# Kernel tuning notes

Measured on AMD Instinct MI355X. Metric: run time of the kernel, lower is better.

Reference implementation:

```python
import jax, jax.numpy as jnp
import numpy as np

N, E, D, H = 50000, 800000, 128, 4
DH = D // H
BN_EPS = 1e-5


def setup_inputs() -> dict:
    key = jax.random.key(0)
    ks = jax.random.split(key, 16)
    s = 0.02
    inp = {
        "x": jax.random.normal(ks[0], (N, D), dtype=jnp.float32),
        "edge_index": jax.random.randint(ks[1], (2, E), 0, N, dtype=jnp.int64),
        "Wk": jax.random.normal(ks[2], (D, D), dtype=jnp.float32) * s,
        "bk": jnp.zeros((D,), jnp.float32),
        "Wm": jax.random.normal(ks[3], (D, D), dtype=jnp.float32) * s,
        "bm": jnp.zeros((D,), jnp.float32),
        "Wq": jax.random.normal(ks[4], (D, D), dtype=jnp.float32) * s,
        "bq": jnp.zeros((D,), jnp.float32),
        "W1": jax.random.normal(ks[5], (D, D), dtype=jnp.float32) * s,
        "b1": jnp.zeros((D,), jnp.float32),
        "gamma": jnp.ones((D,), jnp.float32),
        "beta": jnp.zeros((D,), jnp.float32),
        "W2": jax.random.normal(ks[6], (D, D), dtype=jnp.float32) * s,
        "b2": jnp.zeros((D,), jnp.float32),
    }
    return inp


def reference(x, edge_index, Wk, bk, Wm, bm, Wq, bq, W1, b1, gamma, beta, W2, b2):
    src = edge_index[0]  # [E] softmax segment key
    dst = edge_index[1]  # [E] aggregation target
    x_i = x[dst]         # [E, D] (torch code: X[1])
    x_j = x[src]         # [E, D] (torch code: X[0])

    key = (x_i @ Wk + bk).reshape(-1, H, DH)
    msg = (x_j @ Wm + bm).reshape(-1, H, DH)
    query = (x_j @ Wq + bq).reshape(-1, H, DH) / jnp.sqrt(jnp.float32(DH))

    scores = jnp.sum(query * key, axis=2)  # [E, H]

    # segment softmax over src node index (numerically stable)
    smax = jax.ops.segment_max(scores, src, num_segments=N)
    e = jnp.exp(scores - smax[src])
    ssum = jax.ops.segment_sum(e, src, num_segments=N)
    alpha = e / ssum[src]  # [E, H]

    # rescale by per-src-node edge count
    cnt = jax.ops.segment_sum(jnp.ones((scores.shape[0],), jnp.float32), src, num_segments=N)
    alpha = alpha * cnt[src][:, None]

    out_e = (msg * alpha[:, :, None]).reshape(-1, D)  # [E, D]
    out = jax.ops.segment_sum(out_e, dst, num_segments=N)  # [N, D]

    # MLP: Linear -> BatchNorm1d (training-mode batch stats) -> ReLU -> Linear
    h = out @ W1 + b1
    mean = jnp.mean(h, axis=0)
    var = jnp.var(h, axis=0)  # biased variance, as torch BN uses for normalization
    h = (h - mean) * jax.lax.rsqrt(var + BN_EPS) * gamma + beta
    h = jax.nn.relu(h)
    return h @ W2 + b2
```

## Files before the change

kernel.cpp:

```cpp
#include <hip/hip_runtime.h>
#include <hip/hip_bf16.h>

#define N_NODES 50000
#define N_EDGES 800000
#define DIM 128
#define NHEAD 4
#define GEMM_BLOCKS 782
#define RANK_ILP 8
#define RANK_BLOCKS 391

typedef __bf16 bf16x8 __attribute__((ext_vector_type(8)));
typedef __bf16 bf16x2 __attribute__((ext_vector_type(2)));
typedef float f32x4 __attribute__((ext_vector_type(4)));

struct WPtrs { const float* w[5]; };

__global__ __launch_bounds__(256) void prep_weights(WPtrs P, __bf16* __restrict__ Wt)
{
  __shared__ __bf16 tileT[16][136];
  const int mat = blockIdx.x >> 3, sl = blockIdx.x & 7;
  const float* W = P.w[mat];
  const int col0 = sl * 16;
  const int t = threadIdx.x;
  #pragma unroll
  for (int i = 0; i < 8; ++i) {
    int id = t + i * 256;
    int k = id >> 4, c = id & 15;
    tileT[c][k] = (__bf16)W[k * 128 + col0 + c];
  }
  __syncthreads();
  int c = t >> 4, kb = t & 15;
  bf16x8 v = *(const bf16x8*)&tileT[c][kb * 8];
  *(bf16x8*)&Wt[(size_t)mat * 16384 + (size_t)(col0 + c) * 128 + kb * 8] = v;
}


__device__ __forceinline__ void stage_Wt_half(const __bf16* __restrict__ Wt,
    int half, __bf16 (*wLDS)[136])
{
  const int t = threadIdx.x;
  const __bf16* base = Wt + (size_t)half * 64 * 128;
  #pragma unroll
  for (int i = 0; i < 4; ++i) {
    int id = t + i * 256;
    int col = id >> 4, kb = id & 15;
    bf16x8 v = ((const bf16x8*)(base + (size_t)col * 128))[kb];
    *(bf16x8*)&wLDS[col][kb * 8] = v;
  }
}

__device__ __forceinline__ void stage_A_f32(const float* __restrict__ A, int row0,
    int nrows, __bf16 (*aLDS)[136])
{
  const int t = threadIdx.x;
  #pragma unroll
  for (int i = 0; i < 4; ++i) {
    int id = t + i * 256;
    int r = id >> 4, cb = id & 15;
    int gr = row0 + r;
    float4 v0 = make_float4(0.f, 0.f, 0.f, 0.f), v1 = v0;
    if (gr < nrows) {
      const float4* row = (const float4*)(A + (size_t)gr * DIM);
      v0 = row[cb * 2];
      v1 = row[cb * 2 + 1];
    }
    bf16x8 o;
    o[0] = (__bf16)v0.x; o[1] = (__bf16)v0.y; o[2] = (__bf16)v0.z; o[3] = (__bf16)v0.w;
    o[4] = (__bf16)v1.x; o[5] = (__bf16)v1.y; o[6] = (__bf16)v1.z; o[7] = (__bf16)v1.w;
    *(bf16x8*)&aLDS[r][cb * 8] = o;
  }
}

__device__ __forceinline__ void stage_A_bf16(const __bf16* __restrict__ A, int row0,
    int nrows, __bf16 (*aLDS)[136])
{
  const int t = threadIdx.x;
  #pragma unroll
  for (int i = 0; i < 4; ++i) {
    int id = t + i * 256;
    int r = id >> 4, cb = id & 15;
    int gr = row0 + r;
    bf16x8 v = {};
    if (gr < nrows) v = ((const bf16x8*)(A + (size_t)gr * DIM))[cb];
    *(bf16x8*)&aLDS[r][cb * 8] = v;
  }
}

__device__ __forceinline__ void mfma_half(const __bf16 (*aLDS)[136],
    const __bf16 (*wLDS)[136], int half, f32x4 acc[8])
{
  const int lane = threadIdx.x & 63, wave = threadIdx.x >> 6;
  const int m = lane & 15, q = lane >> 4;
  #pragma unroll
  for (int kt = 0; kt < 4; ++kt) {
    bf16x8 a = *(const bf16x8*)&aLDS[wave * 16 + m][kt * 32 + q * 8];
    #pragma unroll
    for (int ct = 0; ct < 4; ++ct) {
      bf16x8 b = *(const bf16x8*)&wLDS[ct * 16 + m][kt * 32 + q * 8];
      acc[half * 4 + ct] =
          __builtin_amdgcn_mfma_f32_16x16x32_bf16(a, b, acc[half * 4 + ct], 0, 0, 0);
    }
  }
}

template <typename OutT>
__device__ __forceinline__ void store_tile(f32x4 acc[8],
    const float* __restrict__ bias, float scale, OutT* __restrict__ C,
    int row0, int nrows)
{
  const int lane = threadIdx.x & 63, wave = threadIdx.x >> 6;
  const int m = lane & 15, q = lane >> 4;
  #pragma unroll
  for (int j = 0; j < 8; ++j) {
    int col = (j >> 2) * 64 + (j & 3) * 16 + m;
    float bv = bias[col];
    #pragma unroll
    for (int r = 0; r < 4; ++r) {
      int row = row0 + wave * 16 + q * 4 + r;
      if (row < nrows) C[(size_t)row * DIM + col] = (OutT)((acc[j][r] + bv) * scale);
    }
  }
}

__device__ __forceinline__ void gemm_pass(const __bf16 (*aLDS)[136],
    __bf16 (*wLDS)[136], const __bf16* __restrict__ Wt, f32x4 acc[8])
{
  #pragma unroll
  for (int i = 0; i < 8; ++i) acc[i] = (f32x4){0.f, 0.f, 0.f, 0.f};
  stage_Wt_half(Wt, 0, wLDS);
  __syncthreads();
  mfma_half(aLDS, wLDS, 0, acc);
  __syncthreads();
  stage_Wt_half(Wt, 1, wLDS);
  __syncthreads();
  mfma_half(aLDS, wLDS, 1, acc);
}

__global__ __launch_bounds__(256) void fat1(const int* __restrict__ ei,
    int* __restrict__ deg, int2* __restrict__ rank,
    const __bf16* __restrict__ Wt, const float* __restrict__ x,
    const float* __restrict__ bk, const float* __restrict__ bm,
    const float* __restrict__ bq,
    __bf16* __restrict__ Kn, __bf16* __restrict__ Mn, __bf16* __restrict__ Qn)
{
  __shared__ __bf16 aLDS[64][136];
  __shared__ __bf16 wLDS[64][136];
  const int b = blockIdx.x, t = threadIdx.x;

  if (b < RANK_BLOCKS) {
    const int base = b * (256 * RANK_ILP) + t;
    int s[RANK_ILP], d[RANK_ILP], rS[RANK_ILP], rD[RANK_ILP];
    #pragma unroll
    for (int i = 0; i < RANK_ILP; ++i) {
      int e = base + i * 256;
      if (e < N_EDGES) { s[i] = ei[e]; d[i] = ei[N_EDGES + e]; }
    }
    #pragma unroll
    for (int i = 0; i < RANK_ILP; ++i) {
      int e = base + i * 256;
      if (e < N_EDGES) rS[i] = atomicAdd(&deg[s[i]], 1);
    }
    #pragma unroll
    for (int i = 0; i < RANK_ILP; ++i) {
      int e = base + i * 256;
      if (e < N_EDGES) rD[i] = atomicAdd(&deg[N_NODES + d[i]], 1);
    }
    #pragma unroll
    for (int i = 0; i < RANK_ILP; ++i) {
      int e = base + i * 256;
      if (e < N_EDGES) rank[e] = make_int2(rS[i], rD[i]);
    }
  } else {
    const int row0 = (b - RANK_BLOCKS) * 64;
    f32x4 acc[8];
    stage_A_f32(x, row0, N_NODES, aLDS);
    gemm_pass(aLDS, wLDS, Wt, acc);
    store_tile<__bf16>(acc, bk, 1.0f, Kn, row0, N_NODES);
    __syncthreads();
    gemm_pass(aLDS, wLDS, Wt + 16384, acc);
    store_tile<__bf16>(acc, bm, 1.0f, Mn, row0, N_NODES);
    __syncthreads();
    gemm_pass(aLDS, wLDS, Wt + 32768, acc);
    store_tile<__bf16>(acc, bq, 0.17677669529663689f, Qn, row0, N_NODES);
  }
}

__global__ __launch_bounds__(256) void scan_pass1(const int* __restrict__ deg,
    int* __restrict__ bsum, int total)
{
  int i = blockIdx.x * 256 + threadIdx.x;
  int v = (i < total) ? deg[i] : 0;
  __shared__ int s[256];
  s[threadIdx.x] = v; __syncthreads();
  for (int o = 128; o > 0; o >>= 1) {
    if (threadIdx.x < o) s[threadIdx.x] += s[threadIdx.x + o];
    __syncthreads();
  }
  if (threadIdx.x == 0) bsum[blockIdx.x] = s[0];
}

__global__ __launch_bounds__(512) void scan_pass2(int* __restrict__ bsum, int nblocks)
{
  int t = threadIdx.x;
  __shared__ int s[512];
  int v = (t < nblocks) ? bsum[t] : 0;
  s[t] = v; __syncthreads();
  for (int o = 1; o < 512; o <<= 1) {
    int x = (t >= o) ? s[t - o] : 0;
    __syncthreads();
    s[t] += x;
    __syncthreads();
  }
  bsum[t] = s[t] - v;
}

__global__ __launch_bounds__(256) void scan_pass3(const int* __restrict__ deg,
    const int* __restrict__ bsum, int* __restrict__ starts, int total)
{
  int t = threadIdx.x, i = blockIdx.x * 256 + t;
  int v = (i < total) ? deg[i] : 0;
  __shared__ int s[256];
  s[t] = v; __syncthreads();
  for (int o = 1; o < 256; o <<= 1) {
    int x = (t >= o) ? s[t - o] : 0;
    __syncthreads();
    s[t] += x;
    __syncthreads();
  }
  if (i < total) starts[i] = bsum[blockIdx.x] + s[t] - v;
}

__global__ __launch_bounds__(256) void edge_place(const int* __restrict__ ei,
    const int2* __restrict__ rank, const int* __restrict__ starts,
    int* __restrict__ elistS, int2* __restrict__ elistD)
{
  int e = blockIdx.x * 256 + threadIdx.x;
  int src = ei[e], dst = ei[N_EDGES + e];
  int2 r = rank[e];
  int pS = starts[src] + r.x;
  int pD = starts[N_NODES + dst] - N_EDGES + r.y;
  elistS[pS] = dst;
  elistD[pD] = make_int2(src, pS);
}

__global__ __launch_bounds__(256) void src_scores(const int* __restrict__ starts,
    const int* __restrict__ degS, const int* __restrict__ elistS,
    const __bf16* __restrict__ Qn, const __bf16* __restrict__ Kn,
    __bf16* __restrict__ Mn, float* __restrict__ wexp)
{
  const int wave = threadIdx.x >> 6, l = threadIdx.x & 63;
  const int n = blockIdx.x * 4 + wave;
  const int g = l >> 4, il = l & 15;
  const int h = il >> 2;
  const int beg = starts[n], end = beg + degS[n];
  if (beg == end) return;

  bf16x8 q8 = ((const bf16x8*)(Qn + (size_t)n * DIM))[il];
  float wsum = 0.f;

  for (int p0 = beg; p0 < end; p0 += 16) {
    int pp[4], dd[4];
    #pragma unroll
    for (int u = 0; u < 4; ++u) {
      pp[u] = p0 + u * 4 + g;
      dd[u] = elistS[min(pp[u], end - 1)];
    }
    bf16x8 kk[4];
    #pragma unroll
    for (int u = 0; u < 4; ++u)
      kk[u] = ((const bf16x8*)(Kn + (size_t)dd[u] * DIM))[il];
    #pragma unroll
    for (int u = 0; u < 4; ++u) {
      float pr = 0.f;
      #pragma unroll
      for (int j = 0; j < 8; ++j) pr += (float)q8[j] * (float)kk[u][j];
      pr += __shfl_xor(pr, 1);
      pr += __shfl_xor(pr, 2);
      float w = (pp[u] < end) ? __expf(pr) : 0.f;
      wsum += w;
      if ((pp[u] < end) && (il & 3) == 0) wexp[(size_t)pp[u] * NHEAD + h] = w;
    }
  }
  wsum += __shfl_xor(wsum, 16);
  wsum += __shfl_xor(wsum, 32);
  float factor = (float)(end - beg) / wsum;

  float fm = __shfl(factor, (l >> 4) << 2);
  bf16x2* mrow = (bf16x2*)(Mn + (size_t)n * DIM);
  bf16x2 mv = mrow[l];
  mv[0] = (__bf16)((float)mv[0] * fm);
  mv[1] = (__bf16)((float)mv[1] * fm);
  mrow[l] = mv;
}

__global__ __launch_bounds__(256) void dst_aggregate(const int* __restrict__ startsD,
    const int* __restrict__ degD, const int2* __restrict__ elistD,
    const __bf16* __restrict__ Mn, const float* __restrict__ wexp,
    __bf16* __restrict__ agg)
{
  const int wave = threadIdx.x >> 6, l = threadIdx.x & 63;
  const int n = blockIdx.x * 4 + wave;
  const int g = l >> 4, il = l & 15;
  const int h = il >> 2;
  const int beg = startsD[n] - N_EDGES, end = beg + degD[n];

  float acc[8];
  #pragma unroll
  for (int j = 0; j < 8; ++j) acc[j] = 0.f;

  for (int q0 = beg; q0 < end; q0 += 16) {
    int qq[4]; int2 ss[4];
    #pragma unroll
    for (int u = 0; u < 4; ++u) {
      qq[u] = q0 + u * 4 + g;
      ss[u] = elistD[min(qq[u], end - 1)];
    }
    float aa[4];
    #pragma unroll
    for (int u = 0; u < 4; ++u) aa[u] = wexp[(size_t)ss[u].y * NHEAD + h];
    bf16x8 mm[4];
    #pragma unroll
    for (int u = 0; u < 4; ++u)
      mm[u] = ((const bf16x8*)(Mn + (size_t)ss[u].x * DIM))[il];
    #pragma unroll
    for (int u = 0; u < 4; ++u) {
      float av = (qq[u] < end) ? aa[u] : 0.f;
      #pragma unroll
      for (int j = 0; j < 8; ++j) acc[j] += (float)mm[u][j] * av;
    }
  }
  #pragma unroll
  for (int j = 0; j < 8; ++j) {
    acc[j] += __shfl_xor(acc[j], 16);
    acc[j] += __shfl_xor(acc[j], 32);
  }
  if (g == 0) {
    bf16x8 o;
    #pragma unroll
    for (int j = 0; j < 8; ++j) o[j] = (__bf16)acc[j];
    *(bf16x8*)(agg + (size_t)n * DIM + il * 8) = o;
  }
}

__global__ __launch_bounds__(256) void gemm_stats(const __bf16* __restrict__ A,
    const __bf16* __restrict__ Wt, const float* __restrict__ bias,
    __bf16* __restrict__ C, float* __restrict__ colsum, float* __restrict__ colsq)
{
  __shared__ __bf16 aLDS[64][136];
  __shared__ __bf16 wLDS[64][136];
  __shared__ float csum[128], csq[128];
  const int t = threadIdx.x;
  const int row0 = blockIdx.x * 64;

  stage_A_bf16(A, row0, N_NODES, aLDS);
  if (t < 128) { csum[t] = 0.f; csq[t] = 0.f; }
  f32x4 acc[8];
  gemm_pass(aLDS, wLDS, Wt, acc);

  const int lane = t & 63, wave = t >> 6;
  const int m = lane & 15, q = lane >> 4;
  #pragma unroll
  for (int j = 0; j < 8; ++j) {
    int col = (j >> 2) * 64 + (j & 3) * 16 + m;
    float bv = bias[col];
    float s = 0.f, s2 = 0.f;
    #pragma unroll
    for (int r = 0; r < 4; ++r) {
      int row = row0 + wave * 16 + q * 4 + r;
      float hv = acc[j][r] + bv;
      if (row < N_NODES) {
        C[(size_t)row * DIM + col] = (__bf16)hv;
        s += hv; s2 += hv * hv;
      }
    }
    s  += __shfl_xor(s, 16);  s  += __shfl_xor(s, 32);
    s2 += __shfl_xor(s2, 16); s2 += __shfl_xor(s2, 32);
    if (q == 0) {
      atomicAdd(&csum[col], s);
      atomicAdd(&csq[col], s2);
    }
  }
  __syncthreads();
  if (t < 128) {
    atomicAdd(&colsum[t], csum[t]);
    atomicAdd(&colsq[t], csq[t]);
  }
}

__global__ __launch_bounds__(256) void gemm_bn(const __bf16* __restrict__ A,
    const __bf16* __restrict__ Wt, const float* __restrict__ bias,
    float* __restrict__ C, const float* __restrict__ colsum,
    const float* __restrict__ colsq, const float* __restrict__ gamma,
    const float* __restrict__ beta)
{
  __shared__ __bf16 aLDS[64][136];
  __shared__ __bf16 wLDS[64][136];
  __shared__ float sA[128], sB[128];
  const int t = threadIdx.x;
  const int row0 = blockIdx.x * 64;

  if (t < 128) {
    float mean = colsum[t] * (1.0f / N_NODES);
    float var = colsq[t] * (1.0f / N_NODES) - mean * mean;
    float inv = rsqrtf(var + 1e-5f);
    float a = gamma[t] * inv;
    sA[t] = a;
    sB[t] = beta[t] - mean * a;
  }
  __syncthreads();

  {
    const int cb = t & 15;
    float sa[8], sb[8];
    #pragma unroll
    for (int j = 0; j < 8; ++j) { sa[j] = sA[cb * 8 + j]; sb[j] = sB[cb * 8 + j]; }
    #pragma unroll
    for (int i = 0; i < 4; ++i) {
      int id = t + i * 256;
      int r = id >> 4;
      int gr = row0 + r;
      bf16x8 v = {};
      if (gr < N_NODES) v = ((const bf16x8*)(A + (size_t)gr * DIM))[cb];
      bf16x8 o;
      #pragma unroll
      for (int j = 0; j < 8; ++j)
        o[j] = (__bf16)fmaxf((float)v[j] * sa[j] + sb[j], 0.f);
      *(bf16x8*)&aLDS[r][cb * 8] = o;
    }
  }
  f32x4 acc[8];
  gemm_pass(aLDS, wLDS, Wt, acc);
  store_tile<float>(acc, bias, 1.0f, C, row0, N_NODES);
}

extern "C" void kernel_launch(void* const* d_in, const int* in_sizes, int n_in,
                              void* d_out, int out_size, void* d_ws, size_t ws_size,
                              hipStream_t stream) {
  const float* x     = (const float*)d_in[0];
  const int*   ei    = (const int*)d_in[1];
  const float* Wk    = (const float*)d_in[2];
  const float* bk    = (const float*)d_in[3];
  const float* Wm    = (const float*)d_in[4];
  const float* bm    = (const float*)d_in[5];
  const float* Wq    = (const float*)d_in[6];
  const float* bq    = (const float*)d_in[7];
  const float* W1    = (const float*)d_in[8];
  const float* b1    = (const float*)d_in[9];
  const float* gamma = (const float*)d_in[10];
  const float* beta  = (const float*)d_in[11];
  const float* W2    = (const float*)d_in[12];
  const float* b2    = (const float*)d_in[13];

  float* ws = (float*)d_ws;
  const size_t ND  = (size_t)N_NODES * DIM;
  const size_t NDh = ND / 2;
  const size_t EH  = (size_t)N_EDGES * NHEAD;
  const int    N2  = 2 * N_NODES;

  __bf16* Kn   = (__bf16*)ws;
  __bf16* Mn   = (__bf16*)(ws + NDh);
  __bf16* Qn   = (__bf16*)(ws + 2 * NDh);
  __bf16* agg  = (__bf16*)(ws + 3 * NDh);
  __bf16* h1   = (__bf16*)(ws + 4 * NDh);
  float*  wexp = ws + 5 * NDh;
  int2*   rank   = (int2*)(wexp + EH);
  int2*   elistD = rank + N_EDGES;
  int*    elistS = (int*)(elistD + N_EDGES);
  int*    deg    = elistS + N_EDGES;
  float*  colsum = (float*)(deg + N2);
  float*  colsq  = colsum + 128;
  int*    starts = (int*)(colsq + 128);
  int*    bsum   = starts + N2;
  __bf16* Wt     = (__bf16*)(bsum + 512);
  float*  outp   = (float*)d_out;

  hipMemsetAsync(deg, 0, (N2 + 256) * sizeof(int), stream);

  const int scan_blocks = (N2 + 255) / 256;
  const int edge_blocks = N_EDGES / 256;
  const int node_blocks = N_NODES / 4;

  WPtrs wp; wp.w[0] = Wk; wp.w[1] = Wm; wp.w[2] = Wq; wp.w[3] = W1; wp.w[4] = W2;
  prep_weights<<<40, 256, 0, stream>>>(wp, Wt);

  fat1<<<RANK_BLOCKS + GEMM_BLOCKS, 256, 0, stream>>>(
      ei, deg, rank, Wt, x, bk, bm, bq, Kn, Mn, Qn);

  scan_pass1<<<scan_blocks, 256, 0, stream>>>(deg, bsum, N2);
  scan_pass2<<<1, 512, 0, stream>>>(bsum, scan_blocks);
  scan_pass3<<<scan_blocks, 256, 0, stream>>>(deg, bsum, starts, N2);
  edge_place<<<edge_blocks, 256, 0, stream>>>(ei, rank, starts, elistS, elistD);

  src_scores<<<node_blocks, 256, 0, stream>>>(starts, deg, elistS, Qn, Kn, Mn, wexp);
  dst_aggregate<<<node_blocks, 256, 0, stream>>>(starts + N_NODES, deg + N_NODES,
                                                 elistD, Mn, wexp, agg);

  gemm_stats<<<GEMM_BLOCKS, 256, 0, stream>>>(agg, Wt + 3 * 16384, b1, h1,
                                              colsum, colsq);
  gemm_bn<<<GEMM_BLOCKS, 256, 0, stream>>>(h1, Wt + 4 * 16384, b2, outp,
                                           colsum, colsq, gamma, beta);
}
```

Measured before the change: 334.8 us.

## Privatize degree-count atomics per XCC and merge with a combine kernel

Edge degree counting now uses a separate counter array per XCC, read from the hardware register, with relaxed workgroup-scope atomics instead of device-wide atomics. Each stored rank is tagged with its XCC id. A new combine kernel sums the eight partial counts and records each XCC's per-node prefix as a byte, and edge placement adds that prefix back. The aim is to cut cross-die atomic coherence traffic. In exchange it adds an eightfold larger memset, an extra kernel launch and more edge_place loads. The byte prefix assumes per-node degrees below 256, and workgroup-scope atomics shared across a whole XCC rely on the L2 handling them coherently.

```diff
diff --git a/kernel.cpp b/kernel.cpp
--- a/kernel.cpp
+++ b/kernel.cpp
@@ -8,6 +8,7 @@
 #define GEMM_BLOCKS 782
 #define RANK_ILP 8
 #define RANK_BLOCKS 391
+#define N2 (2 * N_NODES)
 
 typedef __bf16 bf16x8 __attribute__((ext_vector_type(8)));
 typedef __bf16 bf16x2 __attribute__((ext_vector_type(2)));
@@ -137,7 +138,7 @@
 }
 
 __global__ __launch_bounds__(256) void fat1(const int* __restrict__ ei,
-    int* __restrict__ deg, int2* __restrict__ rank,
+    int* __restrict__ degx, int2* __restrict__ rank,
     const __bf16* __restrict__ Wt, const float* __restrict__ x,
     const float* __restrict__ bk, const float* __restrict__ bm,
     const float* __restrict__ bq,
@@ -148,6 +149,12 @@
   const int b = blockIdx.x, t = threadIdx.x;
 
   if (b < RANK_BLOCKS) {
+    unsigned xcc;
+    asm volatile("s_getreg_b32 %0, hwreg(HW_REG_XCC_ID)" : "=s"(xcc));
+    xcc &= 7u;
+    int* dg = degx + (size_t)xcc * N2;
+    const int xtag = (int)(xcc << 28);
+
     const int base = b * (256 * RANK_ILP) + t;
     int s[RANK_ILP], d[RANK_ILP], rS[RANK_ILP], rD[RANK_ILP];
     #pragma unroll
@@ -158,17 +165,21 @@
     #pragma unroll
     for (int i = 0; i < RANK_ILP; ++i) {
       int e = base + i * 256;
-      if (e < N_EDGES) rS[i] = atomicAdd(&deg[s[i]], 1);
+      if (e < N_EDGES)
+        rS[i] = __hip_atomic_fetch_add(&dg[s[i]], 1, __ATOMIC_RELAXED,
+                                       __HIP_MEMORY_SCOPE_WORKGROUP);
     }
     #pragma unroll
     for (int i = 0; i < RANK_ILP; ++i) {
       int e = base + i * 256;
-      if (e < N_EDGES) rD[i] = atomicAdd(&deg[N_NODES + d[i]], 1);
+      if (e < N_EDGES)
+        rD[i] = __hip_atomic_fetch_add(&dg[N_NODES + d[i]], 1, __ATOMIC_RELAXED,
+                                       __HIP_MEMORY_SCOPE_WORKGROUP);
     }
     #pragma unroll
     for (int i = 0; i < RANK_ILP; ++i) {
       int e = base + i * 256;
-      if (e < N_EDGES) rank[e] = make_int2(rS[i], rD[i]);
+      if (e < N_EDGES) rank[e] = make_int2(rS[i] | xtag, rD[i] | xtag);
     }
   } else {
     const int row0 = (b - RANK_BLOCKS) * 64;
@@ -185,6 +196,21 @@
   }
 }
 
+__global__ __launch_bounds__(256) void xcd_combine(const int* __restrict__ degx,
+    int* __restrict__ degT, unsigned char* __restrict__ xbase)
+{
+  int i = blockIdx.x * 256 + threadIdx.x;
+  if (i >= N2) return;
+  int s = 0;
+  #pragma unroll
+  for (int x = 0; x < 8; ++x) {
+    int c = degx[(size_t)x * N2 + i];
+    xbase[(size_t)x * N2 + i] = (unsigned char)s;
+    s += c;
+  }
+  degT[i] = s;
+}
+
 __global__ __launch_bounds__(256) void scan_pass1(const int* __restrict__ deg,
     int* __restrict__ bsum, int total)
 {
@@ -232,13 +258,19 @@
 
 __global__ __launch_bounds__(256) void edge_place(const int* __restrict__ ei,
     const int2* __restrict__ rank, const int* __restrict__ starts,
+    const unsigned char* __restrict__ xbase,
     int* __restrict__ elistS, int2* __restrict__ elistD)
 {
   int e = blockIdx.x * 256 + threadIdx.x;
   int src = ei[e], dst = ei[N_EDGES + e];
   int2 r = rank[e];
-  int pS = starts[src] + r.x;
-  int pD = starts[N_NODES + dst] - N_EDGES + r.y;
+  unsigned rx = (unsigned)r.x, ry = (unsigned)r.y;
+  int xs = rx >> 28, xd = ry >> 28;
+  int pS = starts[src] + (int)xbase[(size_t)xs * N2 + src]
+         + (int)(rx & 0x0FFFFFFFu);
+  int pD = starts[N_NODES + dst] - N_EDGES
+         + (int)xbase[(size_t)xd * N2 + N_NODES + dst]
+         + (int)(ry & 0x0FFFFFFFu);
   elistS[pS] = dst;
   elistD[pD] = make_int2(src, pS);
 }
@@ -455,7 +487,6 @@
   const size_t ND  = (size_t)N_NODES * DIM;
   const size_t NDh = ND / 2;
   const size_t EH  = (size_t)N_EDGES * NHEAD;
-  const int    N2  = 2 * N_NODES;
 
   __bf16* Kn   = (__bf16*)ws;
   __bf16* Mn   = (__bf16*)(ws + NDh);
@@ -466,15 +497,17 @@
   int2*   rank   = (int2*)(wexp + EH);
   int2*   elistD = rank + N_EDGES;
   int*    elistS = (int*)(elistD + N_EDGES);
-  int*    deg    = elistS + N_EDGES;
-  float*  colsum = (float*)(deg + N2);
+  int*    degx   = elistS + N_EDGES;
+  float*  colsum = (float*)(degx + 8 * N2);
   float*  colsq  = colsum + 128;
-  int*    starts = (int*)(colsq + 128);
+  int*    degT   = (int*)(colsq + 128);
+  int*    starts = degT + N2;
   int*    bsum   = starts + N2;
-  __bf16* Wt     = (__bf16*)(bsum + 512);
+  unsigned char* xbase = (unsigned char*)(bsum + 512);
+  __bf16* Wt     = (__bf16*)(xbase + 8 * N2);
   float*  outp   = (float*)d_out;
 
-  hipMemsetAsync(deg, 0, (N2 + 256) * sizeof(int), stream);
+  hipMemsetAsync(degx, 0, (8 * N2 + 256) * sizeof(int), stream);
 
   const int scan_blocks = (N2 + 255) / 256;
   const int edge_blocks = N_EDGES / 256;
@@ -484,15 +517,18 @@
   prep_weights<<<40, 256, 0, stream>>>(wp, Wt);
 
   fat1<<<RANK_BLOCKS + GEMM_BLOCKS, 256, 0, stream>>>(
-      ei, deg, rank, Wt, x, bk, bm, bq, Kn, Mn, Qn);
-
-  scan_pass1<<<scan_blocks, 256, 0, stream>>>(deg, bsum, N2);
+      ei, degx, rank, Wt, x, bk, bm, bq, Kn, Mn, Qn);
+
+  xcd_combine<<<scan_blocks, 256, 0, stream>>>(degx, degT, xbase);
+
+  scan_pass1<<<scan_blocks, 256, 0, stream>>>(degT, bsum, N2);
   scan_pass2<<<1, 512, 0, stream>>>(bsum, scan_blocks);
-  scan_pass3<<<scan_blocks, 256, 0, stream>>>(deg, bsum, starts, N2);
-  edge_place<<<edge_blocks, 256, 0, stream>>>(ei, rank, starts, elistS, elistD);
-
-  src_scores<<<node_blocks, 256, 0, stream>>>(starts, deg, elistS, Qn, Kn, Mn, wexp);
-  dst_aggregate<<<node_blocks, 256, 0, stream>>>(starts + N_NODES, deg + N_NODES,
+  scan_pass3<<<scan_blocks, 256, 0, stream>>>(degT, bsum, starts, N2);
+  edge_place<<<edge_blocks, 256, 0, stream>>>(ei, rank, starts, xbase,
+                                              elistS, elistD);
+
+  src_scores<<<node_blocks, 256, 0, stream>>>(starts, degT, elistS, Qn, Kn, Mn, wexp);
+  dst_aggregate<<<node_blocks, 256, 0, stream>>>(starts + N_NODES, degT + N_NODES,
                                                  elistD, Mn, wexp, agg);
 
   gemm_stats<<<GEMM_BLOCKS, 256, 0, stream>>>(agg, Wt + 3 * 16384, b1, h1,
```

Result: no change. 340.3 us (+1.6%).

## Replace global-atomic CSR build with two-level bucketed counting sort

Applied to the files above, without the earlier changes.

Replaces the per-edge global atomic degree counting and rank scheme with a two-level counting sort. Per-block LDS histograms over 256-node buckets feed a bucket scan, and edges are scattered into buckets. A per-bucket kernel then ranks them with shared-memory atomics and writes the CSR lists along with starts and degrees. This aims to remove contended global atomics and the multi-pass global scan, at the cost of extra kernels and an extra pass over the edges. wexp is now indexed by the original edge id, and the bucket staging buffers alias the wexp region.

```diff
diff --git a/kernel.cpp b/kernel.cpp
--- a/kernel.cpp
+++ b/kernel.cpp
@@ -6,8 +6,12 @@
 #define DIM 128
 #define NHEAD 4
 #define GEMM_BLOCKS 782
-#define RANK_ILP 8
-#define RANK_BLOCKS 391
+#define HBLOCKS 313
+#define EPB 2560
+#define NBUCK 196
+#define NBUCK2 392
+#define NODE_PAD 50432
+#define N2 (2 * N_NODES)
 
 typedef __bf16 bf16x8 __attribute__((ext_vector_type(8)));
 typedef __bf16 bf16x2 __attribute__((ext_vector_type(2)));
@@ -137,7 +141,7 @@
 }
 
 __global__ __launch_bounds__(256) void fat1(const int* __restrict__ ei,
-    int* __restrict__ deg, int2* __restrict__ rank,
+    int* __restrict__ hist,
     const __bf16* __restrict__ Wt, const float* __restrict__ x,
     const float* __restrict__ bk, const float* __restrict__ bm,
     const float* __restrict__ bq,
@@ -147,31 +151,23 @@
   __shared__ __bf16 wLDS[64][136];
   const int b = blockIdx.x, t = threadIdx.x;
 
-  if (b < RANK_BLOCKS) {
-    const int base = b * (256 * RANK_ILP) + t;
-    int s[RANK_ILP], d[RANK_ILP], rS[RANK_ILP], rD[RANK_ILP];
-    #pragma unroll
-    for (int i = 0; i < RANK_ILP; ++i) {
-      int e = base + i * 256;
-      if (e < N_EDGES) { s[i] = ei[e]; d[i] = ei[N_EDGES + e]; }
-    }
-    #pragma unroll
-    for (int i = 0; i < RANK_ILP; ++i) {
-      int e = base + i * 256;
-      if (e < N_EDGES) rS[i] = atomicAdd(&deg[s[i]], 1);
-    }
-    #pragma unroll
-    for (int i = 0; i < RANK_ILP; ++i) {
-      int e = base + i * 256;
-      if (e < N_EDGES) rD[i] = atomicAdd(&deg[N_NODES + d[i]], 1);
-    }
-    #pragma unroll
-    for (int i = 0; i < RANK_ILP; ++i) {
-      int e = base + i * 256;
-      if (e < N_EDGES) rank[e] = make_int2(rS[i], rD[i]);
-    }
+  if (b < HBLOCKS) {
+    int* h = (int*)&aLDS[0][0];
+    for (int i = t; i < NBUCK2; i += 256) h[i] = 0;
+    __syncthreads();
+    #pragma unroll
+    for (int i = 0; i < 10; ++i) {
+      int e = b * EPB + i * 256 + t;
+      if (e < N_EDGES) {
+        int s = ei[e], d = ei[N_EDGES + e];
+        atomicAdd(&h[s >> 8], 1);
+        atomicAdd(&h[NBUCK + (d >> 8)], 1);
+      }
+    }
+    __syncthreads();
+    for (int i = t; i < NBUCK2; i += 256) hist[b * NBUCK2 + i] = h[i];
   } else {
-    const int row0 = (b - RANK_BLOCKS) * 64;
+    const int row0 = (b - HBLOCKS) * 64;
     f32x4 acc[8];
     stage_A_f32(x, row0, N_NODES, aLDS);
     gemm_pass(aLDS, wLDS, Wt, acc);
@@ -185,66 +181,126 @@
   }
 }
 
-__global__ __launch_bounds__(256) void scan_pass1(const int* __restrict__ deg,
-    int* __restrict__ bsum, int total)
-{
-  int i = blockIdx.x * 256 + threadIdx.x;
-  int v = (i < total) ? deg[i] : 0;
+__global__ __launch_bounds__(64) void bucket_scan(const int* __restrict__ hist,
+    int* __restrict__ bbase, int* __restrict__ tot)
+{
+  const int b = blockIdx.x, l = threadIdx.x;
+  int run = 0;
+  for (int c = 0; c < 5; ++c) {
+    int idx = c * 64 + l;
+    int v = (idx < HBLOCKS) ? hist[idx * NBUCK2 + b] : 0;
+    int orig = v;
+    #pragma unroll
+    for (int o = 1; o < 64; o <<= 1) {
+      int n = __shfl_up(v, o);
+      if (l >= o) v += n;
+    }
+    if (idx < HBLOCKS) bbase[idx * NBUCK2 + b] = run + v - orig;
+    run += __shfl(v, 63);
+  }
+  if (l == 0) tot[b] = run;
+}
+
+__global__ __launch_bounds__(256) void bucket_starts(const int* __restrict__ tot,
+    int* __restrict__ bstart)
+{
   __shared__ int s[256];
-  s[threadIdx.x] = v; __syncthreads();
-  for (int o = 128; o > 0; o >>= 1) {
-    if (threadIdx.x < o) s[threadIdx.x] += s[threadIdx.x + o];
-    __syncthreads();
-  }
-  if (threadIdx.x == 0) bsum[blockIdx.x] = s[0];
-}
-
-__global__ __launch_bounds__(512) void scan_pass2(int* __restrict__ bsum, int nblocks)
-{
-  int t = threadIdx.x;
-  __shared__ int s[512];
-  int v = (t < nblocks) ? bsum[t] : 0;
-  s[t] = v; __syncthreads();
-  for (int o = 1; o < 512; o <<= 1) {
-    int x = (t >= o) ? s[t - o] : 0;
-    __syncthreads();
-    s[t] += x;
-    __syncthreads();
-  }
-  bsum[t] = s[t] - v;
-}
-
-__global__ __launch_bounds__(256) void scan_pass3(const int* __restrict__ deg,
-    const int* __restrict__ bsum, int* __restrict__ starts, int total)
-{
-  int t = threadIdx.x, i = blockIdx.x * 256 + t;
-  int v = (i < total) ? deg[i] : 0;
-  __shared__ int s[256];
+  const int t = threadIdx.x;
+  int v = (t < NBUCK) ? tot[t] : 0;
   s[t] = v; __syncthreads();
   for (int o = 1; o < 256; o <<= 1) {
-    int x = (t >= o) ? s[t - o] : 0;
-    __syncthreads();
-    s[t] += x;
-    __syncthreads();
-  }
-  if (i < total) starts[i] = bsum[blockIdx.x] + s[t] - v;
-}
-
-__global__ __launch_bounds__(256) void edge_place(const int* __restrict__ ei,
-    const int2* __restrict__ rank, const int* __restrict__ starts,
-    int* __restrict__ elistS, int2* __restrict__ elistD)
-{
-  int e = blockIdx.x * 256 + threadIdx.x;
-  int src = ei[e], dst = ei[N_EDGES + e];
-  int2 r = rank[e];
-  int pS = starts[src] + r.x;
-  int pD = starts[N_NODES + dst] - N_EDGES + r.y;
-  elistS[pS] = dst;
-  elistD[pD] = make_int2(src, pS);
+    int x = (t >= o) ? s[t - o] : 0; __syncthreads();
+    s[t] += x; __syncthreads();
+  }
+  if (t < NBUCK) bstart[t] = s[t] - v;
+  __syncthreads();
+  v = (t < NBUCK) ? tot[NBUCK + t] : 0;
+  s[t] = v; __syncthreads();
+  for (int o = 1; o < 256; o <<= 1) {
+    int x = (t >= o) ? s[t - o] : 0; __syncthreads();
+    s[t] += x; __syncthreads();
+  }
+  if (t < NBUCK) bstart[NBUCK + t] = s[t] - v;
+}
+
+__global__ __launch_bounds__(256) void edge_scatter(const int* __restrict__ ei,
+    const int* __restrict__ bbase, const int* __restrict__ bstart,
+    int2* __restrict__ bucketedS, int2* __restrict__ bucketedD)
+{
+  __shared__ int base[NBUCK2];
+  __shared__ int cur[NBUCK2];
+  const int b = blockIdx.x, t = threadIdx.x;
+  for (int i = t; i < NBUCK2; i += 256) {
+    base[i] = bstart[i] + bbase[b * NBUCK2 + i];
+    cur[i] = 0;
+  }
+  __syncthreads();
+  #pragma unroll
+  for (int i = 0; i < 10; ++i) {
+    int e = b * EPB + i * 256 + t;
+    if (e < N_EDGES) {
+      int s = ei[e], d = ei[N_EDGES + e];
+      int pk = s | (d << 16);
+      int bs = s >> 8, bd = NBUCK + (d >> 8);
+      int lo = atomicAdd(&cur[bs], 1);
+      bucketedS[base[bs] + lo] = make_int2(pk, e);
+      int ld = atomicAdd(&cur[bd], 1);
+      bucketedD[base[bd] + ld] = make_int2(pk, e);
+    }
+  }
+}
+
+__global__ __launch_bounds__(256) void bucket_rank(const int2* __restrict__ bucketedS,
+    const int2* __restrict__ bucketedD, const int* __restrict__ bstart,
+    const int* __restrict__ tot,
+    int2* __restrict__ elistS, int2* __restrict__ elistD,
+    int* __restrict__ starts, int* __restrict__ deg,
+    int* __restrict__ startsD, int* __restrict__ degD)
+{
+  __shared__ int c1[256], ns[256], c2[256];
+  const int b = blockIdx.x, t = threadIdx.x;
+  const bool srcSide = (b < NBUCK);
+  const int bb = srcSide ? b : b - NBUCK;
+  const int seg0 = bstart[b];
+  const int cnt = tot[b];
+  const int2* ent = (srcSide ? bucketedS : bucketedD) + seg0;
+
+  c1[t] = 0; c2[t] = 0;
+  __syncthreads();
+  for (int i = t; i < cnt; i += 256) {
+    unsigned pk = (unsigned)ent[i].x;
+    int ln = (int)(srcSide ? (pk & 0xFFFFu) : (pk >> 16)) - (bb << 8);
+    atomicAdd(&c1[ln], 1);
+  }
+  __syncthreads();
+  ns[t] = c1[t]; __syncthreads();
+  for (int o = 1; o < 256; o <<= 1) {
+    int x = (t >= o) ? ns[t - o] : 0; __syncthreads();
+    ns[t] += x; __syncthreads();
+  }
+  {
+    int node = (bb << 8) + t;
+    int nst = ns[t] - c1[t];
+    if (srcSide) { starts[node] = seg0 + nst; deg[node] = c1[t]; }
+    else         { startsD[node] = seg0 + nst; degD[node] = c1[t]; }
+  }
+  __syncthreads();
+  ns[t] -= c1[t];
+  __syncthreads();
+  for (int i = t; i < cnt; i += 256) {
+    int2 en = ent[i];
+    unsigned pk = (unsigned)en.x;
+    int ln = (int)(srcSide ? (pk & 0xFFFFu) : (pk >> 16)) - (bb << 8);
+    int r = atomicAdd(&c2[ln], 1);
+    int pos = seg0 + ns[ln] + r;
+    int other = (int)(srcSide ? (pk >> 16) : (pk & 0xFFFFu));
+    if (srcSide) elistS[pos] = make_int2(other, en.y);
+    else         elistD[pos] = make_int2(other, en.y);
+  }
 }
 
 __global__ __launch_bounds__(256) void src_scores(const int* __restrict__ starts,
-    const int* __restrict__ degS, const int* __restrict__ elistS,
+    const int* __restrict__ degS, const int2* __restrict__ elistS,
     const __bf16* __restrict__ Qn, const __bf16* __restrict__ Kn,
     __bf16* __restrict__ Mn, float* __restrict__ wexp)
 {
@@ -259,16 +315,16 @@
   float wsum = 0.f;
 
   for (int p0 = beg; p0 < end; p0 += 16) {
-    int pp[4], dd[4];
+    int pp[4]; int2 en[4];
     #pragma unroll
     for (int u = 0; u < 4; ++u) {
       pp[u] = p0 + u * 4 + g;
-      dd[u] = elistS[min(pp[u], end - 1)];
+      en[u] = elistS[min(pp[u], end - 1)];
     }
     bf16x8 kk[4];
     #pragma unroll
     for (int u = 0; u < 4; ++u)
-      kk[u] = ((const bf16x8*)(Kn + (size_t)dd[u] * DIM))[il];
+      kk[u] = ((const bf16x8*)(Kn + (size_t)en[u].x * DIM))[il];
     #pragma unroll
     for (int u = 0; u < 4; ++u) {
       float pr = 0.f;
@@ -278,7 +334,7 @@
       pr += __shfl_xor(pr, 2);
       float w = (pp[u] < end) ? __expf(pr) : 0.f;
       wsum += w;
-      if ((pp[u] < end) && (il & 3) == 0) wexp[(size_t)pp[u] * NHEAD + h] = w;
+      if ((pp[u] < end) && (il & 3) == 0) wexp[(size_t)en[u].y * NHEAD + h] = w;
     }
   }
   wsum += __shfl_xor(wsum, 16);
@@ -302,7 +358,7 @@
   const int n = blockIdx.x * 4 + wave;
   const int g = l >> 4, il = l & 15;
   const int h = il >> 2;
-  const int beg = startsD[n] - N_EDGES, end = beg + degD[n];
+  const int beg = startsD[n], end = beg + degD[n];
 
   float acc[8];
   #pragma unroll
@@ -455,7 +511,6 @@
   const size_t ND  = (size_t)N_NODES * DIM;
   const size_t NDh = ND / 2;
   const size_t EH  = (size_t)N_EDGES * NHEAD;
-  const int    N2  = 2 * N_NODES;
 
   __bf16* Kn   = (__bf16*)ws;
   __bf16* Mn   = (__bf16*)(ws + NDh);
@@ -463,37 +518,42 @@
   __bf16* agg  = (__bf16*)(ws + 3 * NDh);
   __bf16* h1   = (__bf16*)(ws + 4 * NDh);
   float*  wexp = ws + 5 * NDh;
-  int2*   rank   = (int2*)(wexp + EH);
-  int2*   elistD = rank + N_EDGES;
-  int*    elistS = (int*)(elistD + N_EDGES);
-  int*    deg    = elistS + N_EDGES;
-  float*  colsum = (float*)(deg + N2);
+  int2*   bucketedS = (int2*)wexp;
+  int2*   bucketedD = bucketedS + N_EDGES;
+  int2*   elistS = (int2*)(wexp + EH);
+  int2*   elistD = elistS + N_EDGES;
+  int*    hist   = (int*)(elistD + N_EDGES);
+  int*    bbase  = hist + HBLOCKS * NBUCK2;
+  int*    tot    = bbase + HBLOCKS * NBUCK2;
+  int*    bstart = tot + NBUCK2;
+  int*    starts = bstart + NBUCK2;
+  int*    deg    = starts + NODE_PAD;
+  int*    startsD= deg + NODE_PAD;
+  int*    degD   = startsD + NODE_PAD;
+  float*  colsum = (float*)(degD + NODE_PAD);
   float*  colsq  = colsum + 128;
-  int*    starts = (int*)(colsq + 128);
-  int*    bsum   = starts + N2;
-  __bf16* Wt     = (__bf16*)(bsum + 512);
+  __bf16* Wt     = (__bf16*)(colsq + 128);
   float*  outp   = (float*)d_out;
 
-  hipMemsetAsync(deg, 0, (N2 + 256) * sizeof(int), stream);
-
-  const int scan_blocks = (N2 + 255) / 256;
-  const int edge_blocks = N_EDGES / 256;
+  hipMemsetAsync(colsum, 0, 256 * sizeof(float), stream);
+
   const int node_blocks = N_NODES / 4;
 
   WPtrs wp; wp.w[0] = Wk; wp.w[1] = Wm; wp.w[2] = Wq; wp.w[3] = W1; wp.w[4] = W2;
   prep_weights<<<40, 256, 0, stream>>>(wp, Wt);
 
-  fat1<<<RANK_BLOCKS + GEMM_BLOCKS, 256, 0, stream>>>(
-      ei, deg, rank, Wt, x, bk, bm, bq, Kn, Mn, Qn);
-
-  scan_pass1<<<scan_blocks, 256, 0, stream>>>(deg, bsum, N2);
-  scan_pass2<<<1, 512, 0, stream>>>(bsum, scan_blocks);
-  scan_pass3<<<scan_blocks, 256, 0, stream>>>(deg, bsum, starts, N2);
-  edge_place<<<edge_blocks, 256, 0, stream>>>(ei, rank, starts, elistS, elistD);
+  fat1<<<HBLOCKS + GEMM_BLOCKS, 256, 0, stream>>>(
+      ei, hist, Wt, x, bk, bm, bq, Kn, Mn, Qn);
+
+  bucket_scan<<<NBUCK2, 64, 0, stream>>>(hist, bbase, tot);
+  bucket_starts<<<1, 256, 0, stream>>>(tot, bstart);
+  edge_scatter<<<HBLOCKS, 256, 0, stream>>>(ei, bbase, bstart, bucketedS, bucketedD);
+  bucket_rank<<<NBUCK2, 256, 0, stream>>>(bucketedS, bucketedD, bstart, tot,
+                                          elistS, elistD, starts, deg,
+                                          startsD, degD);
 
   src_scores<<<node_blocks, 256, 0, stream>>>(starts, deg, elistS, Qn, Kn, Mn, wexp);
-  dst_aggregate<<<node_blocks, 256, 0, stream>>>(starts + N_NODES, deg + N_NODES,
-                                                 elistD, Mn, wexp, agg);
+  dst_aggregate<<<node_blocks, 256, 0, stream>>>(startsD, degD, elistD, Mn, wexp, agg);
 
   gemm_stats<<<GEMM_BLOCKS, 256, 0, stream>>>(agg, Wt + 3 * 16384, b1, h1,
                                               colsum, colsq);
```

Measured after the change: 292.1 us. 12.8% less time.
